# Kernel optimization log

Hardware: AMD Instinct MI355X
Metric: run time of the kernel (lower is better)

## Reference

```python
import jax, jax.numpy as jnp
import numpy as np

B, M, K = 32, 64, 36
DS, DX, DQ, H = 512, 128, 512, 256


def setup_inputs() -> dict:
    key = jax.random.key(0)
    ks = jax.random.split(key, 11)
    sc = lambda fan_in: 1.0 / np.sqrt(fan_in)
    return {
        "s2": jax.random.normal(ks[0], (B, M, DS), jnp.float32),
        "x0": jax.random.normal(ks[1], (B, K, DX), jnp.float32),
        "q": jax.random.normal(ks[2], (B, DQ), jnp.float32),
        # score MLP: Linear(DS+DX+DQ -> H), ReLU, Linear(H -> 1)
        "score_w1": jax.random.normal(ks[3], (DS + DX + DQ, H), jnp.float32) * sc(DS + DX + DQ),
        "score_b1": jax.random.normal(ks[4], (H,), jnp.float32) * 0.01,
        "score_w2": jax.random.normal(ks[5], (H, 1), jnp.float32) * sc(H),
        "score_b2": jax.random.normal(ks[6], (1,), jnp.float32) * 0.01,
        # h MLP: Linear(DS -> H), ReLU, Linear(H -> DX)
        "h_w1": jax.random.normal(ks[7], (DS, H), jnp.float32) * sc(DS),
        "h_b1": jax.random.normal(ks[8], (H,), jnp.float32) * 0.01,
        "h_w2": jax.random.normal(ks[9], (H, DX), jnp.float32) * sc(H),
        "h_b2": jax.random.normal(ks[10], (DX,), jnp.float32) * 0.01,
    }


def reference(s2, x0, q, score_w1, score_b1, score_w2, score_b2, h_w1, h_b1, h_w2, h_b2):
    ds = s2.shape[-1]
    dx = x0.shape[-1]
    # First score Linear over concat [s_exp, x_exp, q_exp] decomposes into
    # block matmuls (same math as Linear on the concat, no 4D concat tensor).
    w_s = score_w1[:ds]            # (DS, H)
    w_x = score_w1[ds:ds + dx]     # (DX, H)
    w_q = score_w1[ds + dx:]       # (DQ, H)
    pre_s = jnp.einsum('bmd,dh->bmh', s2, w_s)   # (b, m, H)
    pre_x = jnp.einsum('bkd,dh->bkh', x0, w_x)   # (b, k, H)
    pre_q = q @ w_q                              # (b, H)
    hidden = jax.nn.relu(pre_s[:, :, None, :] + pre_x[:, None, :, :]
                         + pre_q[:, None, None, :] + score_b1)  # (b, m, k, H)
    logits = jnp.einsum('bmkh,h->bmk', hidden, score_w2[:, 0]) + score_b2[0]
    att = jax.nn.softmax(logits, axis=1)         # softmax over m
    h_s = jax.nn.relu(s2 @ h_w1 + h_b1) @ h_w2 + h_b2  # (b, m, DX)
    agg = jnp.einsum('bmk,bmf->bkf', att, h_s)   # (b, k, DX)
    return jnp.concatenate([x0, agg], axis=-1)   # (b, k, 2*DX)
```

## Files before the change

kernel.cpp:

```cpp
#include <hip/hip_runtime.h>

#define B_  32
#define M_  64
#define K_  36
#define DS_ 512
#define DX_ 128
#define DQ_ 512
#define H_  256

typedef __attribute__((ext_vector_type(8))) short short8v;
typedef __attribute__((ext_vector_type(4))) float float4v;

#define PK_S2 128
#define PK_W  32
#define PXB   288
#define QPB   32

__global__ __launch_bounds__(512) void kernP(
    const float* __restrict__ s2,
    const float* __restrict__ x0,
    const float* __restrict__ q,
    const float* __restrict__ score_w1,
    const float* __restrict__ score_b1,
    const float* __restrict__ h_w1,
    unsigned short* __restrict__ Apk_h,
    unsigned short* __restrict__ Apk_l,
    unsigned short* __restrict__ Bpk_h,
    unsigned short* __restrict__ Bpk_l,
    float* __restrict__ px,
    float* __restrict__ qpre)
{
    __shared__ float comb[4 * H_];
    const int t   = threadIdx.x;
    const int bid = blockIdx.x;

    if (bid < PK_S2) {
        const int rt = bid;
        const float* src = s2 + (size_t)rt * 16 * DS_;
        unsigned short* dh = Apk_h + (size_t)rt * 8192;
        unsigned short* dl = Apk_l + (size_t)rt * 8192;
        #pragma unroll 4
        for (int j = 0; j < 16; ++j) {
            const int f  = t * 16 + j;
            const int i  = f & 7;
            const int l  = (f >> 3) & 63;
            const int ks = f >> 9;
            const int row = l & 15;
            const int k  = ks * 32 + ((l >> 4) << 2) + (i & 3) + ((i >> 2) << 4);
            const float a = src[(size_t)row * DS_ + k];
            const unsigned u  = __float_as_uint(a);
            const unsigned short hi = (unsigned short)(u >> 16);
            const float res = a - __uint_as_float((unsigned)hi << 16);
            const unsigned short lo =
                (unsigned short)(__float_as_uint(res) >> 16);
            dh[f] = hi; dl[f] = lo;
        }

    } else if (bid < PK_S2 + PK_W) {
        const int wi  = bid - PK_S2;
        const int mat = wi >> 4, nt = wi & 15;
        const float* Wsrc = mat ? h_w1 : score_w1;
        unsigned short* dh = Bpk_h + (size_t)wi * 8192;
        unsigned short* dl = Bpk_l + (size_t)wi * 8192;
        #pragma unroll 4
        for (int j = 0; j < 16; ++j) {
            const int f  = t * 16 + j;
            const int i  = f & 7;
            const int l  = (f >> 3) & 63;
            const int ks = f >> 9;
            const int col = nt * 16 + (l & 15);
            const int k  = ks * 32 + ((l >> 4) << 2) + (i & 3) + ((i >> 2) << 4);
            const float a = Wsrc[(size_t)k * H_ + col];
            const unsigned u  = __float_as_uint(a);
            const unsigned short hi = (unsigned short)(u >> 16);
            const float res = a - __uint_as_float((unsigned)hi << 16);
            const unsigned short lo =
                (unsigned short)(__float_as_uint(res) >> 16);
            dh[f] = hi; dl[f] = lo;
        }

    } else if (bid < PK_S2 + PK_W + PXB) {
        const int tile = bid - (PK_S2 + PK_W);
        const int h    = t & 255;
        const int kh   = __builtin_amdgcn_readfirstlane(t >> 8);
        const float* A  = x0 + (size_t)tile * 4 * DX_ + kh * 64;
        const float* Wp = score_w1 + (size_t)(DS_ + kh * 64) * H_ + h;

        float acc[4];
        #pragma unroll
        for (int r = 0; r < 4; ++r) acc[r] = 0.f;

        #pragma unroll 2
        for (int k = 0; k < 64; k += 4) {
            const float b0 = Wp[(size_t)(k + 0) * H_];
            const float b1 = Wp[(size_t)(k + 1) * H_];
            const float b2 = Wp[(size_t)(k + 2) * H_];
            const float b3 = Wp[(size_t)(k + 3) * H_];
            #pragma unroll
            for (int r = 0; r < 4; ++r) {
                const float4 a = *(const float4*)(A + (size_t)r * DX_ + k);
                acc[r] = fmaf(a.x, b0, acc[r]);
                acc[r] = fmaf(a.y, b1, acc[r]);
                acc[r] = fmaf(a.z, b2, acc[r]);
                acc[r] = fmaf(a.w, b3, acc[r]);
            }
        }
        if (kh) {
            #pragma unroll
            for (int r = 0; r < 4; ++r) comb[r * H_ + h] = acc[r];
        }
        __syncthreads();
        if (!kh) {
            const float b1v = score_b1[h];
            float* dst = px + (size_t)tile * 4 * H_ + h;
            #pragma unroll
            for (int r = 0; r < 4; ++r)
                dst[(size_t)r * H_] = acc[r] + comb[r * H_ + h] + b1v;
        }

    } else {
        const int b  = bid - (PK_S2 + PK_W + PXB);
        const int h  = t & 255;
        const int kh = __builtin_amdgcn_readfirstlane(t >> 8);
        const float* qp = q + (size_t)b * DQ_ + kh * 256;
        const float* wq = score_w1 + (size_t)(DS_ + DX_ + kh * 256) * H_ + h;
        float a0 = 0.f, a1 = 0.f, a2 = 0.f, a3 = 0.f;
        #pragma unroll 2
        for (int d = 0; d < 256; d += 4) {
            const float4 q4 = *(const float4*)(qp + d);
            a0 = fmaf(q4.x, wq[(size_t)(d + 0) * H_], a0);
            a1 = fmaf(q4.y, wq[(size_t)(d + 1) * H_], a1);
            a2 = fmaf(q4.z, wq[(size_t)(d + 2) * H_], a2);
            a3 = fmaf(q4.w, wq[(size_t)(d + 3) * H_], a3);
        }
        const float s = (a0 + a1) + (a2 + a3);
        if (kh) comb[h] = s;
        __syncthreads();
        if (!kh) qpre[(size_t)b * H_ + h] = s + comb[h];
    }
}

__global__ __launch_bounds__(64) void kernG(
    const unsigned short* __restrict__ Apk_h,
    const unsigned short* __restrict__ Apk_l,
    const unsigned short* __restrict__ Bpk_h,
    const unsigned short* __restrict__ Bpk_l,
    const float* __restrict__ h_b1,
    float* __restrict__ pre_s,
    float* __restrict__ h1r)
{
    const int l   = threadIdx.x;
    const int bid = blockIdx.x;
    const int ns  = bid & 7;
    const int mat = (bid >> 3) & 1;
    const int rt  = bid >> 4;

    const short8v* Ah = (const short8v*)Apk_h + (size_t)rt * 16 * 64 + l;
    const short8v* Al = (const short8v*)Apk_l + (size_t)rt * 16 * 64 + l;
    const int nt0 = mat * 16 + ns * 2;
    const short8v* B0h = (const short8v*)Bpk_h + (size_t)nt0 * 16 * 64 + l;
    const short8v* B0l = (const short8v*)Bpk_l + (size_t)nt0 * 16 * 64 + l;
    const short8v* B1h = B0h + 16 * 64;
    const short8v* B1l = B0l + 16 * 64;

    float4v aA0 = {0.f, 0.f, 0.f, 0.f}, aB0 = aA0, aC0 = aA0;
    float4v aA1 = aA0, aB1 = aA0, aC1 = aA0;

    #pragma unroll 2
    for (int ks = 0; ks < 16; ++ks) {
        const short8v ah  = Ah[(size_t)ks * 64];
        const short8v al  = Al[(size_t)ks * 64];
        const short8v b0h = B0h[(size_t)ks * 64];
        const short8v b0l = B0l[(size_t)ks * 64];
        const short8v b1h = B1h[(size_t)ks * 64];
        const short8v b1l = B1l[(size_t)ks * 64];
        aA0 = __builtin_amdgcn_mfma_f32_16x16x32_bf16(ah, b0h, aA0, 0, 0, 0);
        aB0 = __builtin_amdgcn_mfma_f32_16x16x32_bf16(ah, b0l, aB0, 0, 0, 0);
        aC0 = __builtin_amdgcn_mfma_f32_16x16x32_bf16(al, b0h, aC0, 0, 0, 0);
        aA1 = __builtin_amdgcn_mfma_f32_16x16x32_bf16(ah, b1h, aA1, 0, 0, 0);
        aB1 = __builtin_amdgcn_mfma_f32_16x16x32_bf16(ah, b1l, aB1, 0, 0, 0);
        aC1 = __builtin_amdgcn_mfma_f32_16x16x32_bf16(al, b1h, aC1, 0, 0, 0);
    }

    const float4v s0 = aA0 + aB0 + aC0;
    const float4v s1 = aA1 + aB1 + aC1;

    const int row0 = rt * 16 + ((l >> 4) << 2);
    const int c0   = ns * 32 + (l & 15);

    if (!mat) {
        #pragma unroll
        for (int r = 0; r < 4; ++r) {
            pre_s[(size_t)(row0 + r) * H_ + c0]      = s0[r];
            pre_s[(size_t)(row0 + r) * H_ + c0 + 16] = s1[r];
        }
    } else {
        const float bv0 = h_b1[c0];
        const float bv1 = h_b1[c0 + 16];
        #pragma unroll
        for (int r = 0; r < 4; ++r) {
            h1r[(size_t)(row0 + r) * H_ + c0]      = fmaxf(s0[r] + bv0, 0.f);
            h1r[(size_t)(row0 + r) * H_ + c0 + 16] = fmaxf(s1[r] + bv1, 0.f);
        }
    }
}

__global__ __launch_bounds__(256) void kern2(
    const float* __restrict__ h1r,
    const float* __restrict__ h_w2,
    float* __restrict__ hs)
{
    __shared__ float A[4 * H_];
    __shared__ float part[4][DX_];
    const int t  = threadIdx.x;
    const int r0 = blockIdx.x * 4;

    {
        const int flat = t * 4;
        *(float4*)&A[flat] = *(const float4*)(h1r + (size_t)r0 * H_ + flat);
    }
    __syncthreads();

    const int fq  = (t & 31) * 4;
    const int g   = t >> 5;
    const int row = g & 3, kh = g >> 2;
    const float* ap = &A[row * H_ + kh * 128];
    const float* wp = h_w2 + (size_t)(kh * 128) * DX_ + fq;

    float4 acc = {0.f, 0.f, 0.f, 0.f};
    #pragma unroll 4
    for (int d = 0; d < 128; d += 4) {
        const float a0 = ap[d], a1 = ap[d + 1], a2 = ap[d + 2], a3 = ap[d + 3];
        const float4 w0  = *(const float4*)(wp + (size_t)(d + 0) * DX_);
        const float4 w1  = *(const float4*)(wp + (size_t)(d + 1) * DX_);
        const float4 w2v = *(const float4*)(wp + (size_t)(d + 2) * DX_);
        const float4 w3  = *(const float4*)(wp + (size_t)(d + 3) * DX_);
        acc.x = fmaf(a0, w0.x, acc.x); acc.y = fmaf(a0, w0.y, acc.y);
        acc.z = fmaf(a0, w0.z, acc.z); acc.w = fmaf(a0, w0.w, acc.w);
        acc.x = fmaf(a1, w1.x, acc.x); acc.y = fmaf(a1, w1.y, acc.y);
        acc.z = fmaf(a1, w1.z, acc.z); acc.w = fmaf(a1, w1.w, acc.w);
        acc.x = fmaf(a2, w2v.x, acc.x); acc.y = fmaf(a2, w2v.y, acc.y);
        acc.z = fmaf(a2, w2v.z, acc.z); acc.w = fmaf(a2, w2v.w, acc.w);
        acc.x = fmaf(a3, w3.x, acc.x); acc.y = fmaf(a3, w3.y, acc.y);
        acc.z = fmaf(a3, w3.z, acc.z); acc.w = fmaf(a3, w3.w, acc.w);
    }
    if (kh) *(float4*)&part[row][fq] = acc;
    __syncthreads();
    if (!kh) {
        const float4 p = *(const float4*)&part[row][fq];
        float4 o;
        o.x = acc.x + p.x; o.y = acc.y + p.y;
        o.z = acc.z + p.z; o.w = acc.w + p.w;
        *(float4*)(hs + (size_t)(r0 + row) * DX_ + fq) = o;
    }
}

__global__ __launch_bounds__(256) void kern3(
    const float* __restrict__ pre_s,
    const float* __restrict__ px,
    const float* __restrict__ qpre,
    const float* __restrict__ score_w2,
    const float* __restrict__ hs,
    const float* __restrict__ h_b2,
    const float* __restrict__ x0,
    float* __restrict__ out)
{
    __shared__ float logit[M_];
    __shared__ float att[M_];
    __shared__ float pr[DX_];

    const int t    = threadIdx.x;
    const int bk   = blockIdx.x;
    const int b    = bk / K_;
    const int lane = t & 63, wave = t >> 6;
    const int hq   = lane << 2;
    const int f    = t & 127, mh = t >> 7;

    float4 c4, v4;
    {
        const float4 qv = *(const float4*)(qpre + (size_t)b * H_ + hq);
        const float4 pv = *(const float4*)(px + (size_t)bk * H_ + hq);
        c4.x = qv.x + pv.x; c4.y = qv.y + pv.y;
        c4.z = qv.z + pv.z; c4.w = qv.w + pv.w;
        v4 = *(const float4*)(score_w2 + hq);
    }

    float hv[32];
    {
        const float* hsp = hs + ((size_t)b * M_ + mh * 32) * DX_ + f;
        #pragma unroll
        for (int m2 = 0; m2 < 32; ++m2)
            hv[m2] = hsp[(size_t)m2 * DX_];
    }

    const float* ps = pre_s + (size_t)b * M_ * H_;
    #pragma unroll 2
    for (int mi = 0; mi < 16; ++mi) {
        const int m = wave * 16 + mi;
        const float4 p = *(const float4*)(ps + (size_t)m * H_ + hq);
        float x = fmaxf(p.x + c4.x, 0.f) * v4.x
                + fmaxf(p.y + c4.y, 0.f) * v4.y
                + fmaxf(p.z + c4.z, 0.f) * v4.z
                + fmaxf(p.w + c4.w, 0.f) * v4.w;
        #pragma unroll
        for (int off = 32; off > 0; off >>= 1)
            x += __shfl_xor(x, off, 64);
        if (lane == 0) logit[m] = x;
    }
    __syncthreads();

    if (wave == 0) {
        const float L = logit[lane];
        float mx = L;
        #pragma unroll
        for (int off = 32; off > 0; off >>= 1)
            mx = fmaxf(mx, __shfl_xor(mx, off, 64));
        const float e = expf(L - mx);
        float sm = e;
        #pragma unroll
        for (int off = 32; off > 0; off >>= 1)
            sm += __shfl_xor(sm, off, 64);
        att[lane] = e / sm;
    }
    __syncthreads();

    {
        float r = 0.f;
        #pragma unroll
        for (int m2 = 0; m2 < 32; ++m2)
            r = fmaf(att[mh * 32 + m2], hv[m2], r);
        if (mh) pr[f] = r;
        __syncthreads();
        if (!mh)
            out[(size_t)bk * (2 * DX_) + DX_ + f] = r + pr[f] + h_b2[f];
    }
    if (t < DX_)
        out[(size_t)bk * (2 * DX_) + t] = x0[(size_t)bk * DX_ + t];
}

extern "C" void kernel_launch(void* const* d_in, const int* in_sizes, int n_in,
                              void* d_out, int out_size, void* d_ws, size_t ws_size,
                              hipStream_t stream) {
    (void)in_sizes; (void)n_in; (void)out_size; (void)ws_size;
    const float* s2       = (const float*)d_in[0];
    const float* x0       = (const float*)d_in[1];
    const float* q        = (const float*)d_in[2];
    const float* score_w1 = (const float*)d_in[3];
    const float* score_b1 = (const float*)d_in[4];
    const float* score_w2 = (const float*)d_in[5];
    const float* h_w1     = (const float*)d_in[7];
    const float* h_b1     = (const float*)d_in[8];
    const float* h_w2     = (const float*)d_in[9];
    const float* h_b2     = (const float*)d_in[10];
    float* out = (float*)d_out;

    float* ws    = (float*)d_ws;
    float* pre_s = ws;
    float* h1r   = pre_s + (size_t)B_ * M_ * H_;
    float* px    = h1r   + (size_t)B_ * M_ * H_;
    float* qpre  = px    + (size_t)B_ * K_ * H_;
    float* hs    = qpre  + (size_t)B_ * H_;

    unsigned short* Apk_h = (unsigned short*)(ws + 2097152);
    unsigned short* Apk_l = Apk_h + (size_t)128 * 16 * 64 * 8;
    unsigned short* Bpk_h = Apk_l + (size_t)128 * 16 * 64 * 8;
    unsigned short* Bpk_l = Bpk_h + (size_t)32 * 16 * 64 * 8;

    kernP<<<PK_S2 + PK_W + PXB + QPB, 512, 0, stream>>>(
        s2, x0, q, score_w1, score_b1, h_w1,
        Apk_h, Apk_l, Bpk_h, Bpk_l, px, qpre);
    kernG<<<2048, 64, 0, stream>>>(Apk_h, Apk_l, Bpk_h, Bpk_l, h_b1,
                                   pre_s, h1r);
    kern2<<<512, 256, 0, stream>>>(h1r, h_w2, hs);
    kern3<<<B_ * K_, 256, 0, stream>>>(pre_s, px, qpre, score_w2, hs, h_b2,
                                       x0, out);
}
```

Baseline: 119.4 us.

## Stage bf16-split packing through LDS with coalesced vector loads and stores

```diff
diff --git a/kernel.cpp b/kernel.cpp
--- a/kernel.cpp
+++ b/kernel.cpp
@@ -11,10 +11,19 @@
 typedef __attribute__((ext_vector_type(8))) short short8v;
 typedef __attribute__((ext_vector_type(4))) float float4v;
 
-#define PK_S2 128
-#define PK_W  32
-#define PXB   288
-#define QPB   32
+#define APK 256
+#define BPK 32
+#define PXB 288
+#define QPB 32
+
+__device__ __forceinline__ void bfsplit(float a, unsigned short* h,
+                                        unsigned short* s) {
+    const unsigned u = __float_as_uint(a);
+    const unsigned short hi = (unsigned short)(u >> 16);
+    const float r = a - __uint_as_float((unsigned)hi << 16);
+    *h = hi;
+    *s = (unsigned short)(__float_as_uint(r) >> 16);
+}
 
 __global__ __launch_bounds__(512) void kernP(
     const float* __restrict__ s2,
@@ -30,57 +39,89 @@
     float* __restrict__ px,
     float* __restrict__ qpre)
 {
+    __shared__ float stage[8192];
     __shared__ float comb[4 * H_];
     const int t   = threadIdx.x;
     const int bid = blockIdx.x;
 
-    if (bid < PK_S2) {
-        const int rt = bid;
-        const float* src = s2 + (size_t)rt * 16 * DS_;
-        unsigned short* dh = Apk_h + (size_t)rt * 8192;
-        unsigned short* dl = Apk_l + (size_t)rt * 8192;
-        #pragma unroll 4
-        for (int j = 0; j < 16; ++j) {
-            const int f  = t * 16 + j;
-            const int i  = f & 7;
-            const int l  = (f >> 3) & 63;
-            const int ks = f >> 9;
-            const int row = l & 15;
-            const int k  = ks * 32 + ((l >> 4) << 2) + (i & 3) + ((i >> 2) << 4);
-            const float a = src[(size_t)row * DS_ + k];
-            const unsigned u  = __float_as_uint(a);
-            const unsigned short hi = (unsigned short)(u >> 16);
-            const float res = a - __uint_as_float((unsigned)hi << 16);
-            const unsigned short lo =
-                (unsigned short)(__float_as_uint(res) >> 16);
-            dh[f] = hi; dl[f] = lo;
-        }
-
-    } else if (bid < PK_S2 + PK_W) {
-        const int wi  = bid - PK_S2;
-        const int mat = wi >> 4, nt = wi & 15;
+    if (bid < APK) {
+        const int rt = bid >> 1, half = bid & 1;
+        const float* src = s2 + (size_t)rt * 16 * DS_ + half * 256;
+
+        #pragma unroll
+        for (int i2 = 0; i2 < 2; ++i2) {
+            const int f2 = t * 4 + i2 * 2048;
+            *(float4*)&stage[f2] =
+                *(const float4*)(src + (size_t)(f2 >> 8) * DS_ + (f2 & 255));
+        }
+        __syncthreads();
+
+        const int base = (t & 15) * 256 + (t >> 6) * 32 + (((t >> 4) & 3) << 2);
+        const float4 a0 = *(const float4*)&stage[base];
+        const float4 a1 = *(const float4*)&stage[base + 16];
+        const float va[8] = {a0.x, a0.y, a0.z, a0.w, a1.x, a1.y, a1.z, a1.w};
+
+        unsigned int oh[4], ol[4];
+        #pragma unroll
+        for (int p = 0; p < 4; ++p) {
+            unsigned short h0, s0, h1, s1;
+            bfsplit(va[2 * p],     &h0, &s0);
+            bfsplit(va[2 * p + 1], &h1, &s1);
+            oh[p] = (unsigned)h0 | ((unsigned)h1 << 16);
+            ol[p] = (unsigned)s0 | ((unsigned)s1 << 16);
+        }
+        const size_t dst = (size_t)rt * 4096 + half * 2048 + t * 4;
+        *(uint4*)((unsigned int*)Apk_h + dst) =
+            make_uint4(oh[0], oh[1], oh[2], oh[3]);
+        *(uint4*)((unsigned int*)Apk_l + dst) =
+            make_uint4(ol[0], ol[1], ol[2], ol[3]);
+
+    } else if (bid < APK + BPK) {
+        const int bw = bid - APK;
+        const int ks = bw & 15, mat = bw >> 4;
         const float* Wsrc = mat ? h_w1 : score_w1;
-        unsigned short* dh = Bpk_h + (size_t)wi * 8192;
-        unsigned short* dl = Bpk_l + (size_t)wi * 8192;
-        #pragma unroll 4
-        for (int j = 0; j < 16; ++j) {
-            const int f  = t * 16 + j;
-            const int i  = f & 7;
-            const int l  = (f >> 3) & 63;
-            const int ks = f >> 9;
+
+        #pragma unroll
+        for (int i2 = 0; i2 < 4; ++i2) {
+            const int f2 = t * 4 + i2 * 2048;
+            *(float4*)&stage[f2] = *(const float4*)(
+                Wsrc + (size_t)(ks * 32 + (f2 >> 8)) * H_ + (f2 & 255));
+        }
+        __syncthreads();
+
+        const int nt = t >> 5;
+        const int lA = (t * 2) & 63;
+        unsigned int oh[8], ol[8];
+        #pragma unroll
+        for (int jl = 0; jl < 2; ++jl) {
+            const int l   = lA + jl;
             const int col = nt * 16 + (l & 15);
-            const int k  = ks * 32 + ((l >> 4) << 2) + (i & 3) + ((i >> 2) << 4);
-            const float a = Wsrc[(size_t)k * H_ + col];
-            const unsigned u  = __float_as_uint(a);
-            const unsigned short hi = (unsigned short)(u >> 16);
-            const float res = a - __uint_as_float((unsigned)hi << 16);
-            const unsigned short lo =
-                (unsigned short)(__float_as_uint(res) >> 16);
-            dh[f] = hi; dl[f] = lo;
-        }
-
-    } else if (bid < PK_S2 + PK_W + PXB) {
-        const int tile = bid - (PK_S2 + PK_W);
+            const int kb  = (l >> 4) << 2;
+            #pragma unroll
+            for (int p = 0; p < 4; ++p) {
+                const int i0  = 2 * p, i1 = 2 * p + 1;
+                const int kk0 = kb + (i0 & 3) + ((i0 >> 2) << 4);
+                const int kk1 = kb + (i1 & 3) + ((i1 >> 2) << 4);
+                unsigned short h0, s0, h1, s1;
+                bfsplit(stage[kk0 * 256 + col], &h0, &s0);
+                bfsplit(stage[kk1 * 256 + col], &h1, &s1);
+                oh[jl * 4 + p] = (unsigned)h0 | ((unsigned)h1 << 16);
+                ol[jl * 4 + p] = (unsigned)s0 | ((unsigned)s1 << 16);
+            }
+        }
+        const size_t dst =
+            (size_t)(mat * 16 + nt) * 4096 + ks * 256 + (size_t)lA * 4;
+        *(uint4*)((unsigned int*)Bpk_h + dst) =
+            make_uint4(oh[0], oh[1], oh[2], oh[3]);
+        *(uint4*)((unsigned int*)Bpk_h + dst + 4) =
+            make_uint4(oh[4], oh[5], oh[6], oh[7]);
+        *(uint4*)((unsigned int*)Bpk_l + dst) =
+            make_uint4(ol[0], ol[1], ol[2], ol[3]);
+        *(uint4*)((unsigned int*)Bpk_l + dst + 4) =
+            make_uint4(ol[4], ol[5], ol[6], ol[7]);
+
+    } else if (bid < APK + BPK + PXB) {
+        const int tile = bid - (APK + BPK);
         const int h    = t & 255;
         const int kh   = __builtin_amdgcn_readfirstlane(t >> 8);
         const float* A  = x0 + (size_t)tile * 4 * DX_ + kh * 64;
@@ -119,7 +160,7 @@
         }
 
     } else {
-        const int b  = bid - (PK_S2 + PK_W + PXB);
+        const int b  = bid - (APK + BPK + PXB);
         const int h  = t & 255;
         const int kh = __builtin_amdgcn_readfirstlane(t >> 8);
         const float* qp = q + (size_t)b * DQ_ + kh * 256;
@@ -366,7 +407,7 @@
     unsigned short* Bpk_h = Apk_l + (size_t)128 * 16 * 64 * 8;
     unsigned short* Bpk_l = Bpk_h + (size_t)32 * 16 * 64 * 8;
 
-    kernP<<<PK_S2 + PK_W + PXB + QPB, 512, 0, stream>>>(
+    kernP<<<APK + BPK + PXB + QPB, 512, 0, stream>>>(
         s2, x0, q, score_w1, score_b1, h_w1,
         Apk_h, Apk_l, Bpk_h, Bpk_l, px, qpre);
     kernG<<<2048, 64, 0, stream>>>(Apk_h, Apk_l, Bpk_h, Bpk_l, h_b1,
```

Measured after the change: 120.8 us. Within noise of the previous version (+1.2%).

## Fuse h-MLP second layer into MFMA GEMM kernel via shared-memory tile

Applied to the files above, without the earlier changes.

```diff
diff --git a/kernel.cpp b/kernel.cpp
--- a/kernel.cpp
+++ b/kernel.cpp
@@ -140,20 +140,24 @@
     }
 }
 
-__global__ __launch_bounds__(64) void kernG(
+__global__ __launch_bounds__(512) void kernG2(
     const unsigned short* __restrict__ Apk_h,
     const unsigned short* __restrict__ Apk_l,
     const unsigned short* __restrict__ Bpk_h,
     const unsigned short* __restrict__ Bpk_l,
     const float* __restrict__ h_b1,
+    const float* __restrict__ h_w2,
     float* __restrict__ pre_s,
-    float* __restrict__ h1r)
+    float* __restrict__ hs)
 {
-    const int l   = threadIdx.x;
+    __shared__ float hre[16 * 264];
+
+    const int t   = threadIdx.x;
+    const int l   = t & 63;
+    const int ns  = __builtin_amdgcn_readfirstlane(t >> 6);
     const int bid = blockIdx.x;
-    const int ns  = bid & 7;
-    const int mat = (bid >> 3) & 1;
-    const int rt  = bid >> 4;
+    const int mat = bid & 1;
+    const int rt  = bid >> 1;
 
     const short8v* Ah = (const short8v*)Apk_h + (size_t)rt * 16 * 64 + l;
     const short8v* Al = (const short8v*)Apk_l + (size_t)rt * 16 * 64 + l;
@@ -185,10 +189,11 @@
     const float4v s0 = aA0 + aB0 + aC0;
     const float4v s1 = aA1 + aB1 + aC1;
 
-    const int row0 = rt * 16 + ((l >> 4) << 2);
-    const int c0   = ns * 32 + (l & 15);
+    const int rl0 = (l >> 4) << 2;
+    const int c0  = ns * 32 + (l & 15);
 
     if (!mat) {
+        const int row0 = rt * 16 + rl0;
         #pragma unroll
         for (int r = 0; r < 4; ++r) {
             pre_s[(size_t)(row0 + r) * H_ + c0]      = s0[r];
@@ -199,59 +204,26 @@
         const float bv1 = h_b1[c0 + 16];
         #pragma unroll
         for (int r = 0; r < 4; ++r) {
-            h1r[(size_t)(row0 + r) * H_ + c0]      = fmaxf(s0[r] + bv0, 0.f);
-            h1r[(size_t)(row0 + r) * H_ + c0 + 16] = fmaxf(s1[r] + bv1, 0.f);
-        }
-    }
-}
-
-__global__ __launch_bounds__(256) void kern2(
-    const float* __restrict__ h1r,
-    const float* __restrict__ h_w2,
-    float* __restrict__ hs)
-{
-    __shared__ float A[4 * H_];
-    __shared__ float part[4][DX_];
-    const int t  = threadIdx.x;
-    const int r0 = blockIdx.x * 4;
-
-    {
-        const int flat = t * 4;
-        *(float4*)&A[flat] = *(const float4*)(h1r + (size_t)r0 * H_ + flat);
-    }
-    __syncthreads();
-
-    const int fq  = (t & 31) * 4;
-    const int g   = t >> 5;
-    const int row = g & 3, kh = g >> 2;
-    const float* ap = &A[row * H_ + kh * 128];
-    const float* wp = h_w2 + (size_t)(kh * 128) * DX_ + fq;
-
-    float4 acc = {0.f, 0.f, 0.f, 0.f};
-    #pragma unroll 4
-    for (int d = 0; d < 128; d += 4) {
-        const float a0 = ap[d], a1 = ap[d + 1], a2 = ap[d + 2], a3 = ap[d + 3];
-        const float4 w0  = *(const float4*)(wp + (size_t)(d + 0) * DX_);
-        const float4 w1  = *(const float4*)(wp + (size_t)(d + 1) * DX_);
-        const float4 w2v = *(const float4*)(wp + (size_t)(d + 2) * DX_);
-        const float4 w3  = *(const float4*)(wp + (size_t)(d + 3) * DX_);
-        acc.x = fmaf(a0, w0.x, acc.x); acc.y = fmaf(a0, w0.y, acc.y);
-        acc.z = fmaf(a0, w0.z, acc.z); acc.w = fmaf(a0, w0.w, acc.w);
-        acc.x = fmaf(a1, w1.x, acc.x); acc.y = fmaf(a1, w1.y, acc.y);
-        acc.z = fmaf(a1, w1.z, acc.z); acc.w = fmaf(a1, w1.w, acc.w);
-        acc.x = fmaf(a2, w2v.x, acc.x); acc.y = fmaf(a2, w2v.y, acc.y);
-        acc.z = fmaf(a2, w2v.z, acc.z); acc.w = fmaf(a2, w2v.w, acc.w);
-        acc.x = fmaf(a3, w3.x, acc.x); acc.y = fmaf(a3, w3.y, acc.y);
-        acc.z = fmaf(a3, w3.z, acc.z); acc.w = fmaf(a3, w3.w, acc.w);
-    }
-    if (kh) *(float4*)&part[row][fq] = acc;
-    __syncthreads();
-    if (!kh) {
-        const float4 p = *(const float4*)&part[row][fq];
-        float4 o;
-        o.x = acc.x + p.x; o.y = acc.y + p.y;
-        o.z = acc.z + p.z; o.w = acc.w + p.w;
-        *(float4*)(hs + (size_t)(r0 + row) * DX_ + fq) = o;
+            hre[(rl0 + r) * 264 + c0]      = fmaxf(s0[r] + bv0, 0.f);
+            hre[(rl0 + r) * 264 + c0 + 16] = fmaxf(s1[r] + bv1, 0.f);
+        }
+        __syncthreads();
+
+        const int g  = t >> 5;
+        const int fq = (t & 31) * 4;
+        const float* w2p = h_w2 + fq;
+        const float* hr  = &hre[g * 264];
+        float4 acc = {0.f, 0.f, 0.f, 0.f};
+        #pragma unroll 4
+        for (int k = 0; k < H_; ++k) {
+            const float  hvv = hr[k];
+            const float4 w4  = *(const float4*)(w2p + (size_t)k * DX_);
+            acc.x = fmaf(hvv, w4.x, acc.x);
+            acc.y = fmaf(hvv, w4.y, acc.y);
+            acc.z = fmaf(hvv, w4.z, acc.z);
+            acc.w = fmaf(hvv, w4.w, acc.w);
+        }
+        *(float4*)(hs + ((size_t)rt * 16 + g) * DX_ + fq) = acc;
     }
 }
 
@@ -356,8 +328,7 @@
 
     float* ws    = (float*)d_ws;
     float* pre_s = ws;
-    float* h1r   = pre_s + (size_t)B_ * M_ * H_;
-    float* px    = h1r   + (size_t)B_ * M_ * H_;
+    float* px    = pre_s + (size_t)B_ * M_ * H_;
     float* qpre  = px    + (size_t)B_ * K_ * H_;
     float* hs    = qpre  + (size_t)B_ * H_;
 
@@ -369,9 +340,8 @@
     kernP<<<PK_S2 + PK_W + PXB + QPB, 512, 0, stream>>>(
         s2, x0, q, score_w1, score_b1, h_w1,
         Apk_h, Apk_l, Bpk_h, Bpk_l, px, qpre);
-    kernG<<<2048, 64, 0, stream>>>(Apk_h, Apk_l, Bpk_h, Bpk_l, h_b1,
-                                   pre_s, h1r);
-    kern2<<<512, 256, 0, stream>>>(h1r, h_w2, hs);
+    kernG2<<<256, 512, 0, stream>>>(Apk_h, Apk_l, Bpk_h, Bpk_l, h_b1, h_w2,
+                                    pre_s, hs);
     kern3<<<B_ * K_, 256, 0, stream>>>(pre_s, px, qpre, score_w2, hs, h_b2,
                                        x0, out);
 }
```

Result: slower. 128.9 us (+8.0%).
